# Kernel tuning notes

Measured on AMD Instinct MI355X. Metric: run time of the kernel, lower is better.

## Reference

```python
import jax, jax.numpy as jnp
from jax import lax
import numpy as np

D = 1024      # hidden_size
H = 6         # num_heads
DK = 128      # head_k_dim
DV = 256      # head_v_dim (head_dim * expand_v)
KD = H * DK   # key_dim = 768
VD = H * DV   # value_dim = 1536
KS = 4        # conv_size
EPS = 1e-5
B, L = 2, 1024


def _causal_conv_silu(x, w):
    # x: [B, L, C], w: [C, KS] depthwise causal conv then SiLU
    xt = jnp.transpose(x, (0, 2, 1))  # [B, C, L]
    out = lax.conv_general_dilated(
        xt, w[:, None, :], window_strides=(1,), padding=[(KS - 1, 0)],
        feature_group_count=w.shape[0])
    return jnp.transpose(jax.nn.silu(out), (0, 2, 1))  # [B, L, C]


def setup_inputs() -> dict:
    key = jax.random.key(0)
    ks = jax.random.split(key, 16)
    s = 0.02
    x = jax.random.normal(ks[0], (B, L, D), dtype=jnp.float32)
    Wq = jax.random.normal(ks[1], (D, KD), dtype=jnp.float32) * s
    Wk = jax.random.normal(ks[2], (D, KD), dtype=jnp.float32) * s
    Wv = jax.random.normal(ks[3], (D, VD), dtype=jnp.float32) * s
    Wb = jax.random.normal(ks[4], (D, H), dtype=jnp.float32) * s
    Wa = jax.random.normal(ks[5], (D, H), dtype=jnp.float32) * s
    A_log = jnp.log(jax.random.uniform(ks[6], (H,), minval=1e-3, maxval=16.0))
    dt = jnp.exp(jax.random.uniform(ks[7], (H,)) * (np.log(0.1) - np.log(0.001)) + np.log(0.001))
    dt = jnp.clip(dt, 1e-4)
    dt_bias = dt + jnp.log(-jnp.expm1(-dt))
    conv_q = jax.random.normal(ks[8], (KD, KS), dtype=jnp.float32) * 0.3
    conv_k = jax.random.normal(ks[9], (KD, KS), dtype=jnp.float32) * 0.3
    conv_v = jax.random.normal(ks[10], (VD, KS), dtype=jnp.float32) * 0.3
    Wg = jax.random.normal(ks[11], (D, VD), dtype=jnp.float32) * s
    norm_w = jnp.ones((DV,), dtype=jnp.float32)
    Wo = jax.random.normal(ks[12], (VD, D), dtype=jnp.float32) * s
    return {"x": x, "Wq": Wq, "Wk": Wk, "Wv": Wv, "Wb": Wb, "Wa": Wa,
            "A_log": A_log, "dt_bias": dt_bias, "conv_q": conv_q,
            "conv_k": conv_k, "conv_v": conv_v, "Wg": Wg,
            "norm_w": norm_w, "Wo": Wo}


def _l2norm(t):
    return t * lax.rsqrt(jnp.sum(t * t, axis=-1, keepdims=True) + 1e-12)


def reference(x, Wq, Wk, Wv, Wb, Wa, A_log, dt_bias, conv_q, conv_k, conv_v,
              Wg, norm_w, Wo):
    Bc, Lc, _ = x.shape
    q = _causal_conv_silu(x @ Wq, conv_q).reshape(Bc, Lc, H, DK)
    k = _causal_conv_silu(x @ Wk, conv_k).reshape(Bc, Lc, H, DK)
    v = _causal_conv_silu(x @ Wv, conv_v).reshape(Bc, Lc, H, DV)
    beta = jax.nn.sigmoid(x @ Wb)                              # [B,L,H]
    g = -jnp.exp(A_log) * jax.nn.softplus(x @ Wa + dt_bias)     # [B,L,H]

    q = _l2norm(q) * (DK ** -0.5)
    k = _l2norm(k)

    # time-major for scan
    qt = jnp.moveaxis(q, 1, 0)    # [L,B,H,DK]
    kt = jnp.moveaxis(k, 1, 0)
    vt = jnp.moveaxis(v, 1, 0)    # [L,B,H,DV]
    gt = jnp.moveaxis(g, 1, 0)    # [L,B,H]
    bt = jnp.moveaxis(beta, 1, 0)

    S0 = jnp.zeros((Bc, H, DK, DV), dtype=x.dtype)

    def step(S, inp):
        q_t, k_t, v_t, g_t, b_t = inp
        S = S * jnp.exp(g_t)[..., None, None]
        corr = jnp.einsum('bhk,bhkv->bhv', k_t, S)
        u = (v_t - corr) * b_t[..., None]
        S = S + k_t[..., None] * u[:, :, None, :]
        o_t = jnp.einsum('bhk,bhkv->bhv', q_t, S)
        return S, o_t

    S, o = lax.scan(step, S0, (qt, kt, vt, gt, bt))
    o = jnp.moveaxis(o, 0, 1)      # [B,L,H,DV]

    gate = (x @ Wg).reshape(Bc, Lc, H, DV)
    o = o * lax.rsqrt(jnp.mean(o * o, axis=-1, keepdims=True) + EPS)
    o = o * norm_w * jax.nn.silu(gate)
    o = o.reshape(Bc, Lc, VD) @ Wo
    return o, S
```

## Files before the change

kernel.cpp:

```cpp
#include <hip/hip_runtime.h>

#define B_ 2
#define L_ 1024
#define D_ 1024
#define H_ 6
#define DK_ 128
#define DV_ 256
#define KD_ 768
#define VD_ 1536
#define KS_ 4
#define KD2_ 1536
#define VD2_ 3072

using bf16x8 = __attribute__((ext_vector_type(8))) short;
using u16x8 = __attribute__((ext_vector_type(8))) unsigned short;
using f32x4 = __attribute__((ext_vector_type(4))) float;

__device__ __forceinline__ float silu_f(float x) { return x / (1.0f + expf(-x)); }

__device__ __forceinline__ unsigned short f2bf(float f) {
  unsigned int u = __float_as_uint(f);
  u = (u + 0x7fffu + ((u >> 16) & 1u)) >> 16;
  return (unsigned short)u;
}

__device__ __forceinline__ void gl_lds16(const void* g, void* l) {
  __builtin_amdgcn_global_load_lds((const __attribute__((address_space(1))) unsigned int*)g,
                                   (__attribute__((address_space(3))) unsigned int*)l, 16, 0, 0);
}
__device__ __forceinline__ void gl_lds4(const void* g, void* l) {
  __builtin_amdgcn_global_load_lds((const __attribute__((address_space(1))) unsigned int*)g,
                                   (__attribute__((address_space(3))) unsigned int*)l, 4, 0, 0);
}

template <int CTRL>
__device__ __forceinline__ float dpp_add(float x) {
  int y = __builtin_amdgcn_mov_dpp(__float_as_int(x), CTRL, 0xF, 0xF, true);
  return x + __int_as_float(y);
}
__device__ __forceinline__ float red16(float x) {
  x = dpp_add<0xB1>(x);
  x = dpp_add<0x4E>(x);
  x = dpp_add<0x141>(x);
  x = dpp_add<0x140>(x);
  return x;
}

__global__ __launch_bounds__(256) void sgemm64(const float* __restrict__ A,
                                               const float* __restrict__ Bm,
                                               float* __restrict__ C,
                                               int M, int N, int K) {
  __shared__ float As[16][64];
  __shared__ float Bs[16][64];
  const int tid = threadIdx.x;
  const int bx = blockIdx.x, by = blockIdx.y;
  const int tx = tid & 15, ty = tid >> 4;
  const int m0 = by * 64, n0 = bx * 64;
  const int ar = tid >> 2, ac = (tid & 3) << 2;
  const int br = tid >> 4, bc = (tid & 15) << 2;
  const bool n4 = ((N & 3) == 0);
  float acc[4][4];
#pragma unroll
  for (int i = 0; i < 4; i++)
#pragma unroll
    for (int j = 0; j < 4; j++) acc[i][j] = 0.0f;

  for (int k0 = 0; k0 < K; k0 += 16) {
    float4 av = *reinterpret_cast<const float4*>(A + (size_t)(m0 + ar) * K + (k0 + ac));
    As[ac + 0][ar] = av.x;
    As[ac + 1][ar] = av.y;
    As[ac + 2][ar] = av.z;
    As[ac + 3][ar] = av.w;
    float4 bv;
    if (n4 && (n0 + bc + 3 < N)) {
      bv = *reinterpret_cast<const float4*>(Bm + (size_t)(k0 + br) * N + (n0 + bc));
    } else {
      bv.x = (n0 + bc + 0 < N) ? Bm[(size_t)(k0 + br) * N + (n0 + bc + 0)] : 0.0f;
      bv.y = (n0 + bc + 1 < N) ? Bm[(size_t)(k0 + br) * N + (n0 + bc + 1)] : 0.0f;
      bv.z = (n0 + bc + 2 < N) ? Bm[(size_t)(k0 + br) * N + (n0 + bc + 2)] : 0.0f;
      bv.w = (n0 + bc + 3 < N) ? Bm[(size_t)(k0 + br) * N + (n0 + bc + 3)] : 0.0f;
    }
    Bs[br][bc + 0] = bv.x;
    Bs[br][bc + 1] = bv.y;
    Bs[br][bc + 2] = bv.z;
    Bs[br][bc + 3] = bv.w;
    __syncthreads();
#pragma unroll
    for (int kk = 0; kk < 16; kk++) {
      float4 a = *reinterpret_cast<const float4*>(&As[kk][ty << 2]);
      float4 b = *reinterpret_cast<const float4*>(&Bs[kk][tx << 2]);
      acc[0][0] = fmaf(a.x, b.x, acc[0][0]);
      acc[0][1] = fmaf(a.x, b.y, acc[0][1]);
      acc[0][2] = fmaf(a.x, b.z, acc[0][2]);
      acc[0][3] = fmaf(a.x, b.w, acc[0][3]);
      acc[1][0] = fmaf(a.y, b.x, acc[1][0]);
      acc[1][1] = fmaf(a.y, b.y, acc[1][1]);
      acc[1][2] = fmaf(a.y, b.z, acc[1][2]);
      acc[1][3] = fmaf(a.y, b.w, acc[1][3]);
      acc[2][0] = fmaf(a.z, b.x, acc[2][0]);
      acc[2][1] = fmaf(a.z, b.y, acc[2][1]);
      acc[2][2] = fmaf(a.z, b.z, acc[2][2]);
      acc[2][3] = fmaf(a.z, b.w, acc[2][3]);
      acc[3][0] = fmaf(a.w, b.x, acc[3][0]);
      acc[3][1] = fmaf(a.w, b.y, acc[3][1]);
      acc[3][2] = fmaf(a.w, b.z, acc[3][2]);
      acc[3][3] = fmaf(a.w, b.w, acc[3][3]);
    }
    __syncthreads();
  }
#pragma unroll
  for (int i = 0; i < 4; i++) {
    int m = m0 + (ty << 2) + i;
#pragma unroll
    for (int j = 0; j < 4; j++) {
      int n = n0 + (tx << 2) + j;
      if (n < N) C[(size_t)m * N + n] = acc[i][j];
    }
  }
}

__global__ void cast_bf16_kernel(const float* __restrict__ in, unsigned short* __restrict__ out,
                                 int n4) {
  int i = blockIdx.x * 256 + threadIdx.x;
  if (i >= n4) return;
  float4 v = *reinterpret_cast<const float4*>(in + (size_t)i * 4);
  ushort4 o;
  o.x = f2bf(v.x);
  o.y = f2bf(v.y);
  o.z = f2bf(v.z);
  o.w = f2bf(v.w);
  *reinterpret_cast<ushort4*>(out + (size_t)i * 4) = o;
}

__global__ __launch_bounds__(256) void tcast_kernel(const float* __restrict__ W,
                                                    unsigned short* __restrict__ Wt,
                                                    int K, int N) {
  __shared__ unsigned short T[64][72];
  const int tid = threadIdx.x;
  const int k0 = blockIdx.y * 64, n0 = blockIdx.x * 64;
  const int c4 = (tid & 15) * 4, r = tid >> 4;
#pragma unroll
  for (int j = 0; j < 4; j++) {
    int row = r + j * 16;
    float4 w = *reinterpret_cast<const float4*>(W + (size_t)(k0 + row) * N + n0 + c4);
    T[c4 + 0][row] = f2bf(w.x);
    T[c4 + 1][row] = f2bf(w.y);
    T[c4 + 2][row] = f2bf(w.z);
    T[c4 + 3][row] = f2bf(w.w);
  }
  __syncthreads();
#pragma unroll
  for (int j = 0; j < 4; j++) {
    int nr = r + j * 16;
    ushort4 o;
    o.x = T[nr][c4 + 0];
    o.y = T[nr][c4 + 1];
    o.z = T[nr][c4 + 2];
    o.w = T[nr][c4 + 3];
    *reinterpret_cast<ushort4*>(Wt + (size_t)(n0 + nr) * K + k0 + c4) = o;
  }
}

__global__ __launch_bounds__(256) void mfma_gemm(const unsigned short* __restrict__ A,
                                                 const unsigned short* __restrict__ Bt,
                                                 float* __restrict__ C,
                                                 int M, int N, int K) {
  __shared__ __attribute__((aligned(16))) unsigned short As[128][32];
  __shared__ __attribute__((aligned(16))) unsigned short Bs[128][32];
  const int tid = threadIdx.x;
  const int wave = tid >> 6, lane = tid & 63;
  const int wm = wave >> 1, wn = wave & 1;
  const int m0 = blockIdx.y * 128, n0 = blockIdx.x * 128;
  const int lrow = lane >> 4;
  const int lcol = lane & 15;
  const int sr = lane >> 2;
  const int sc = lane & 3;

  f32x4 acc[4][4];
#pragma unroll
  for (int i = 0; i < 4; i++)
#pragma unroll
    for (int j = 0; j < 4; j++) acc[i][j] = f32x4{0.f, 0.f, 0.f, 0.f};

  const int Ra = wave * 32;

  for (int k0 = 0; k0 < K; k0 += 32) {
#pragma unroll
    for (int half = 0; half < 2; half++) {
      int r = Ra + half * 16 + sr;
      int ch = sc ^ ((r >> 1) & 3);
      gl_lds16(A + (size_t)(m0 + r) * K + k0 + ch * 8, &As[Ra + half * 16][0]);
      gl_lds16(Bt + (size_t)(n0 + r) * K + k0 + ch * 8, &Bs[Ra + half * 16][0]);
    }
    __syncthreads();
    bf16x8 af[4], bfr[4];
#pragma unroll
    for (int mr = 0; mr < 4; mr++) {
      int row = wm * 64 + mr * 16 + lcol;
      af[mr] = *reinterpret_cast<const bf16x8*>(&As[row][(lrow ^ ((row >> 1) & 3)) * 8]);
    }
#pragma unroll
    for (int nr = 0; nr < 4; nr++) {
      int row = wn * 64 + nr * 16 + lcol;
      bfr[nr] = *reinterpret_cast<const bf16x8*>(&Bs[row][(lrow ^ ((row >> 1) & 3)) * 8]);
    }
#pragma unroll
    for (int mr = 0; mr < 4; mr++)
#pragma unroll
      for (int nr = 0; nr < 4; nr++)
        acc[mr][nr] = __builtin_amdgcn_mfma_f32_16x16x32_bf16(af[mr], bfr[nr], acc[mr][nr], 0, 0, 0);
    __syncthreads();
  }

#pragma unroll
  for (int mr = 0; mr < 4; mr++) {
    int row = m0 + wm * 64 + mr * 16 + lrow * 4;
#pragma unroll
    for (int nr = 0; nr < 4; nr++) {
      int col = n0 + wn * 64 + nr * 16 + lcol;
#pragma unroll
      for (int r = 0; r < 4; r++) C[(size_t)(row + r) * N + col] = acc[mr][nr][r];
    }
  }
}

__global__ void concat_ba_kernel(const float* __restrict__ Wb, const float* __restrict__ Wa,
                                 float* __restrict__ Wba) {
  int i = blockIdx.x * 256 + threadIdx.x;
  if (i >= D_ * 12) return;
  int k = i / 12, j = i % 12;
  Wba[i] = (j < 6) ? Wb[k * 6 + j] : Wa[k * 6 + (j - 6)];
}

__global__ void ba_kernel(const float* __restrict__ yba,
                          const float* __restrict__ A_log, const float* __restrict__ dt_bias,
                          float* __restrict__ beta_t, float* __restrict__ eg_t) {
  int i = blockIdx.x * 256 + threadIdx.x;
  if (i >= B_ * L_ * H_) return;
  int h = i % H_, bl = i / H_;
  int l = bl % L_, b = bl / L_;
  float yb = yba[(size_t)bl * 12 + h];
  float ya = yba[(size_t)bl * 12 + 6 + h];
  float beta = 1.0f / (1.0f + expf(-yb));
  float z = ya + dt_bias[h];
  float sp = (z > 20.0f) ? z : log1pf(expf(z));
  float g = -expf(A_log[h]) * sp;
  size_t o = ((size_t)b * H_ + h) * L_ + l;
  beta_t[o] = beta;
  eg_t[o] = expf(g);
}

__global__ __launch_bounds__(256) void conv_qk_kernel(
    const float* __restrict__ yqk,
    const float* __restrict__ cwq, const float* __restrict__ cwk,
    float* __restrict__ qhat, float* __restrict__ khat) {
  const int lane = threadIdx.x & 63;
  const int widx = (blockIdx.x << 2) + (threadIdx.x >> 6);
  const int h = widx % H_;
  const int bl = widx / H_;
  const int l = bl % L_;
  const int b = bl / L_;
  const int ch = lane << 1;
  const int gc = h * DK_ + ch;

  float wq0[KS_], wq1[KS_], wk0[KS_], wk1[KS_];
#pragma unroll
  for (int j = 0; j < KS_; j++) {
    wq0[j] = cwq[(size_t)gc * KS_ + j];
    wq1[j] = cwq[(size_t)(gc + 1) * KS_ + j];
    wk0[j] = cwk[(size_t)gc * KS_ + j];
    wk1[j] = cwk[(size_t)(gc + 1) * KS_ + j];
  }
  float aq0 = 0, aq1 = 0, ak0 = 0, ak1 = 0;
#pragma unroll
  for (int j = 0; j < KS_; j++) {
    int ll = l - (KS_ - 1) + j;
    if (ll >= 0) {
      const size_t off = (size_t)(b * L_ + ll) * KD2_ + gc;
      float2 tq = *reinterpret_cast<const float2*>(yqk + off);
      float2 tk = *reinterpret_cast<const float2*>(yqk + off + 768);
      aq0 = fmaf(tq.x, wq0[j], aq0);
      aq1 = fmaf(tq.y, wq1[j], aq1);
      ak0 = fmaf(tk.x, wk0[j], ak0);
      ak1 = fmaf(tk.y, wk1[j], ak1);
    }
  }
  float q0 = silu_f(aq0), q1 = silu_f(aq1);
  float k0v = silu_f(ak0), k1v = silu_f(ak1);
  float ssq = q0 * q0 + q1 * q1;
  float ssk = k0v * k0v + k1v * k1v;
#pragma unroll
  for (int m = 1; m < 64; m <<= 1) {
    ssq += __shfl_xor(ssq, m);
    ssk += __shfl_xor(ssk, m);
  }
  float xq = ssq + 1e-12f;
  float rq = rsqrtf(xq);
  rq = rq * (1.5f - 0.5f * xq * rq * rq);
  float xk = ssk + 1e-12f;
  float rk = rsqrtf(xk);
  rk = rk * (1.5f - 0.5f * xk * rk * rk);
  rq *= 0.08838834764831845f;
  size_t oo = (size_t)bl * KD_ + gc;
  *reinterpret_cast<float2*>(qhat + oo) = make_float2(q0 * rq, q1 * rq);
  *reinterpret_cast<float2*>(khat + oo) = make_float2(k0v * rk, k1v * rk);
}

__global__ void conv_v_kernel(const float* __restrict__ yvg, const float* __restrict__ cwv,
                              float* __restrict__ v) {
  int idx = blockIdx.x * 256 + threadIdx.x;
  int c = idx % VD_;
  int bl = idx / VD_;
  int l = bl % L_;
  float w[KS_];
#pragma unroll
  for (int j = 0; j < KS_; j++) w[j] = cwv[(size_t)c * KS_ + j];
  float acc = 0;
#pragma unroll
  for (int j = 0; j < KS_; j++) {
    int ll = l - (KS_ - 1) + j;
    if (ll >= 0) acc = fmaf(yvg[(size_t)(bl - l + ll) * VD2_ + c], w[j], acc);
  }
  v[idx] = silu_f(acc);
}

__global__ __launch_bounds__(256) void gp_kernel(const float* __restrict__ qhat,
                                                 const float* __restrict__ khat,
                                                 float* __restrict__ gp) {
  const int W = (blockIdx.x << 2) + (threadIdx.x >> 6);
  const int lane = threadIdx.x & 63;
  const int blk = W & 255;
  const int bh = W >> 8;
  const int b = bh / H_, h = bh % H_;
  const int t0 = blk * 4;
  const size_t base = (size_t)(b * L_ + t0) * KD_ + h * DK_ + 2 * lane;
  float2 k1 = *reinterpret_cast<const float2*>(khat + base);
  float2 k2 = *reinterpret_cast<const float2*>(khat + base + KD_);
  float2 k3 = *reinterpret_cast<const float2*>(khat + base + 2 * KD_);
  float2 k4 = *reinterpret_cast<const float2*>(khat + base + 3 * KD_);
  float2 q1 = *reinterpret_cast<const float2*>(qhat + base);
  float2 q2 = *reinterpret_cast<const float2*>(qhat + base + KD_);
  float2 q3 = *reinterpret_cast<const float2*>(qhat + base + 2 * KD_);
  float2 q4 = *reinterpret_cast<const float2*>(qhat + base + 3 * KD_);
  float g21 = k2.x * k1.x + k2.y * k1.y;
  float g31 = k3.x * k1.x + k3.y * k1.y;
  float g32 = k3.x * k2.x + k3.y * k2.y;
  float g41 = k4.x * k1.x + k4.y * k1.y;
  float g42 = k4.x * k2.x + k4.y * k2.y;
  float g43 = k4.x * k3.x + k4.y * k3.y;
  float p21 = q2.x * k1.x + q2.y * k1.y;
  float p31 = q3.x * k1.x + q3.y * k1.y;
  float p32 = q3.x * k2.x + q3.y * k2.y;
  float p41 = q4.x * k1.x + q4.y * k1.y;
  float p42 = q4.x * k2.x + q4.y * k2.y;
  float p43 = q4.x * k3.x + q4.y * k3.y;
  float p11 = q1.x * k1.x + q1.y * k1.y;
  float p22 = q2.x * k2.x + q2.y * k2.y;
  float p33 = q3.x * k3.x + q3.y * k3.y;
  float p44 = q4.x * k4.x + q4.y * k4.y;
#pragma unroll
  for (int m = 1; m < 64; m <<= 1) {
    g21 += __shfl_xor(g21, m); g31 += __shfl_xor(g31, m); g32 += __shfl_xor(g32, m);
    g41 += __shfl_xor(g41, m); g42 += __shfl_xor(g42, m); g43 += __shfl_xor(g43, m);
    p21 += __shfl_xor(p21, m); p31 += __shfl_xor(p31, m); p32 += __shfl_xor(p32, m);
    p41 += __shfl_xor(p41, m); p42 += __shfl_xor(p42, m); p43 += __shfl_xor(p43, m);
    p11 += __shfl_xor(p11, m); p22 += __shfl_xor(p22, m); p33 += __shfl_xor(p33, m);
    p44 += __shfl_xor(p44, m);
  }
  const bool l0 = lane & 1, l1 = lane & 2, l2 = lane & 4, l3 = lane & 8;
  float s00 = l0 ? g31 : g21, s01 = l0 ? g41 : g32, s02 = l0 ? g43 : g42, s03 = l0 ? p31 : p21;
  float s04 = l0 ? p41 : p32, s05 = l0 ? p43 : p42, s06 = l0 ? p22 : p11, s07 = l0 ? p44 : p33;
  float s10 = l1 ? s01 : s00, s11 = l1 ? s03 : s02, s12 = l1 ? s05 : s04, s13 = l1 ? s07 : s06;
  float s20 = l2 ? s11 : s10, s21 = l2 ? s13 : s12;
  float out = l3 ? s21 : s20;
  if (lane < 16) gp[((size_t)bh * 256 + blk) * 16 + lane] = out;
}

__global__ __launch_bounds__(64) void scan_kernel(
    const float* __restrict__ qhat, const float* __restrict__ khat,
    const float* __restrict__ vconv, const float* __restrict__ beta_t,
    const float* __restrict__ eg_t, const float* __restrict__ gp,
    float* __restrict__ o_scan, float* __restrict__ S_out) {
  __shared__ __attribute__((aligned(16))) float kq[2][16][256];
  __shared__ __attribute__((aligned(16))) float scv[2][16][4];
  __shared__ __attribute__((aligned(16))) float sce[2][4][16];
  __shared__ __attribute__((aligned(16))) float gps[2][4][16];

  const int lane = threadIdx.x & 63;
  const int wg = blockIdx.x;
  const int virt = (wg & 7) * 96 + (wg >> 3);
  const int bh = virt >> 6;
  const int tile = virt & 63;
  const int b = bh / H_, h = bh % H_;
  const int grp = lane >> 4;
  const int lsub = lane & 15;
  const int col = tile * 4 + grp;

  const float* kbase = khat + (size_t)b * L_ * KD_ + h * DK_;
  const float* qbase = qhat + (size_t)b * L_ * KD_ + h * DK_;
  const float* vbase = vconv + (size_t)b * L_ * VD_ + h * DV_ + tile * 4;
  const float* egp = eg_t + (size_t)bh * L_;
  const float* bp = beta_t + (size_t)bh * L_;
  const float* gpb = gp + (size_t)bh * 256 * 16;
  float* op = o_scan + (size_t)b * L_ * VD_ + h * DV_ + col;

  float S[8];
#pragma unroll
  for (int i = 0; i < 8; i++) S[i] = 0.0f;

  const int sl = lane & 31;
  const int vt = lane >> 2, vc = lane & 3;
  const int et = lane & 15, ej = lane >> 4;
  const float* ebase = (ej == 0) ? egp : bp;

#define STAGE(W, BB)                                                                   \
  do {                                                                                 \
    const int _t0 = (W) * 16;                                                          \
    _Pragma("unroll") for (int _j = 0; _j < 16; _j++) {                                \
      const float* _src = (lane < 32) ? (kbase + (size_t)(_t0 + _j) * KD_ + sl * 4)    \
                                      : (qbase + (size_t)(_t0 + _j) * KD_ + sl * 4);   \
      gl_lds16(_src, &kq[BB][_j][0]);                                                  \
    }                                                                                  \
    gl_lds4(vbase + (size_t)(_t0 + vt) * VD_ + vc, &scv[BB][0][0]);                    \
    gl_lds4(ebase + _t0 + et, &sce[BB][0][0]);                                         \
    gl_lds4(gpb + (size_t)(W) * 64 + lane, &gps[BB][0][0]);                            \
  } while (0)

#define DOT8(L4, H4) \
  ((fmaf(S[0], (L4).x, S[1] * (L4).y) + fmaf(S[2], (L4).z, S[3] * (L4).w)) + \
   (fmaf(S[4], (H4).x, S[5] * (H4).y) + fmaf(S[6], (H4).z, S[7] * (H4).w)))

  STAGE(0, 0);
  STAGE(1, 1);
  asm volatile("s_waitcnt vmcnt(19)" ::: "memory");
  __builtin_amdgcn_sched_barrier(0);

  int cur = 0;
  for (int w = 0; w < L_ / 16; ++w) {
    const int t0 = w * 16;
#pragma unroll
    for (int sb = 0; sb < 4; ++sb) {
      const int j0 = sb * 4;
      float4 k1l = *reinterpret_cast<const float4*>(&kq[cur][j0 + 0][lsub * 4]);
      float4 k1h = *reinterpret_cast<const float4*>(&kq[cur][j0 + 0][64 + lsub * 4]);
      float4 q1l = *reinterpret_cast<const float4*>(&kq[cur][j0 + 0][128 + lsub * 4]);
      float4 q1h = *reinterpret_cast<const float4*>(&kq[cur][j0 + 0][192 + lsub * 4]);
      float4 k2l = *reinterpret_cast<const float4*>(&kq[cur][j0 + 1][lsub * 4]);
      float4 k2h = *reinterpret_cast<const float4*>(&kq[cur][j0 + 1][64 + lsub * 4]);
      float4 q2l = *reinterpret_cast<const float4*>(&kq[cur][j0 + 1][128 + lsub * 4]);
      float4 q2h = *reinterpret_cast<const float4*>(&kq[cur][j0 + 1][192 + lsub * 4]);
      float4 k3l = *reinterpret_cast<const float4*>(&kq[cur][j0 + 2][lsub * 4]);
      float4 k3h = *reinterpret_cast<const float4*>(&kq[cur][j0 + 2][64 + lsub * 4]);
      float4 q3l = *reinterpret_cast<const float4*>(&kq[cur][j0 + 2][128 + lsub * 4]);
      float4 q3h = *reinterpret_cast<const float4*>(&kq[cur][j0 + 2][192 + lsub * 4]);
      float4 k4l = *reinterpret_cast<const float4*>(&kq[cur][j0 + 3][lsub * 4]);
      float4 k4h = *reinterpret_cast<const float4*>(&kq[cur][j0 + 3][64 + lsub * 4]);
      float4 q4l = *reinterpret_cast<const float4*>(&kq[cur][j0 + 3][128 + lsub * 4]);
      float4 q4h = *reinterpret_cast<const float4*>(&kq[cur][j0 + 3][192 + lsub * 4]);
      float v1 = scv[cur][j0 + 0][grp], v2 = scv[cur][j0 + 1][grp];
      float v3 = scv[cur][j0 + 2][grp], v4 = scv[cur][j0 + 3][grp];
      float e1 = sce[cur][0][j0 + 0], e2 = sce[cur][0][j0 + 1];
      float e3 = sce[cur][0][j0 + 2], e4 = sce[cur][0][j0 + 3];
      float bt1 = sce[cur][1][j0 + 0], bt2 = sce[cur][1][j0 + 1];
      float bt3 = sce[cur][1][j0 + 2], bt4 = sce[cur][1][j0 + 3];
      float g21 = gps[cur][sb][0], g31 = gps[cur][sb][1], g32 = gps[cur][sb][2];
      float g41 = gps[cur][sb][3], g42 = gps[cur][sb][4], g43 = gps[cur][sb][5];
      float p21 = gps[cur][sb][6], p31 = gps[cur][sb][7], p32 = gps[cur][sb][8];
      float p41 = gps[cur][sb][9], p42 = gps[cur][sb][10], p43 = gps[cur][sb][11];
      float p11 = gps[cur][sb][12], p22 = gps[cur][sb][13];
      float p33 = gps[cur][sb][14], p44 = gps[cur][sb][15];

      float a1 = red16(DOT8(k1l, k1h));
      float a2 = red16(DOT8(k2l, k2h));
      float a3 = red16(DOT8(k3l, k3h));
      float a4 = red16(DOT8(k4l, k4h));
      float b1 = red16(DOT8(q1l, q1h));
      float b2 = red16(DOT8(q2l, q2h));
      float b3 = red16(DOT8(q3l, q3h));
      float b4 = red16(DOT8(q4l, q4h));

      float E2 = e1 * e2, E3 = E2 * e3, E4 = E3 * e4;
      float f32v = e3 * e2, f43 = e4 * e3, f432 = e4 * f32v;
      float u1 = (v1 - e1 * a1) * bt1;
      float c2 = fmaf(g21, u1, e1 * a2);
      float u2 = (v2 - e2 * c2) * bt2;
      float c3 = fmaf(g32, u2, fmaf(e2 * g31, u1, E2 * a3));
      float u3 = (v3 - e3 * c3) * bt3;
      float c4 = fmaf(g43, u3, fmaf(e3 * g42, u2, fmaf(f32v * g41, u1, E3 * a4)));
      float u4 = (v4 - e4 * c4) * bt4;
      float o1 = fmaf(p11, u1, e1 * b1);
      float o2 = fmaf(p22, u2, fmaf(e2 * p21, u1, E2 * b2));
      float o3 = fmaf(p33, u3, fmaf(e3 * p32, u2, fmaf(f32v * p31, u1, E3 * b3)));
      float o4 = fmaf(p44, u4,
                      fmaf(e4 * p43, u3, fmaf(f43 * p42, u2, fmaf(f432 * p41, u1, E4 * b4))));
      float w1 = f432 * u1, w2 = f43 * u2, w3 = e4 * u3, w4 = u4;

      S[0] = fmaf(k4l.x, w4, fmaf(k3l.x, w3, fmaf(k2l.x, w2, fmaf(k1l.x, w1, S[0] * E4))));
      S[1] = fmaf(k4l.y, w4, fmaf(k3l.y, w3, fmaf(k2l.y, w2, fmaf(k1l.y, w1, S[1] * E4))));
      S[2] = fmaf(k4l.z, w4, fmaf(k3l.z, w3, fmaf(k2l.z, w2, fmaf(k1l.z, w1, S[2] * E4))));
      S[3] = fmaf(k4l.w, w4, fmaf(k3l.w, w3, fmaf(k2l.w, w2, fmaf(k1l.w, w1, S[3] * E4))));
      S[4] = fmaf(k4h.x, w4, fmaf(k3h.x, w3, fmaf(k2h.x, w2, fmaf(k1h.x, w1, S[4] * E4))));
      S[5] = fmaf(k4h.y, w4, fmaf(k3h.y, w3, fmaf(k2h.y, w2, fmaf(k1h.y, w1, S[5] * E4))));
      S[6] = fmaf(k4h.z, w4, fmaf(k3h.z, w3, fmaf(k2h.z, w2, fmaf(k1h.z, w1, S[6] * E4))));
      S[7] = fmaf(k4h.w, w4, fmaf(k3h.w, w3, fmaf(k2h.w, w2, fmaf(k1h.w, w1, S[7] * E4))));

      if (lsub == 0) {
        op[(size_t)(t0 + j0 + 0) * VD_] = o1;
        op[(size_t)(t0 + j0 + 1) * VD_] = o2;
        op[(size_t)(t0 + j0 + 2) * VD_] = o3;
        op[(size_t)(t0 + j0 + 3) * VD_] = o4;
      }
    }
    __builtin_amdgcn_sched_barrier(0);
    if (w < L_ / 16 - 2) {
      STAGE(w + 2, cur);
      asm volatile("s_waitcnt vmcnt(35)" ::: "memory");
    } else {
      asm volatile("s_waitcnt vmcnt(0)" ::: "memory");
    }
    __builtin_amdgcn_sched_barrier(0);
    cur ^= 1;
  }

#pragma unroll
  for (int i = 0; i < 4; i++) {
    S_out[((size_t)bh * DK_ + lsub * 4 + i) * DV_ + col] = S[i];
    S_out[((size_t)bh * DK_ + 64 + lsub * 4 + i) * DV_ + col] = S[4 + i];
  }
#undef STAGE
#undef DOT8
}

__global__ __launch_bounds__(256) void normgate_kernel(
    const float* __restrict__ o_scan, const float* __restrict__ yvg,
    const float* __restrict__ norm_w, unsigned short* __restrict__ o2b) {
  const int lane = threadIdx.x & 63;
  const int widx = (blockIdx.x << 2) + (threadIdx.x >> 6);
  const int h = widx % H_;
  const int bl = widx / H_;
  size_t base = (size_t)bl * VD_ + h * DV_ + (lane << 2);
  size_t gbase = (size_t)bl * VD2_ + VD_ + h * DV_ + (lane << 2);
  float4 o4 = *reinterpret_cast<const float4*>(o_scan + base);
  float ss = o4.x * o4.x + o4.y * o4.y + o4.z * o4.z + o4.w * o4.w;
#pragma unroll
  for (int m = 1; m < 64; m <<= 1) ss += __shfl_xor(ss, m);
  float x = ss * (1.0f / DV_) + 1e-5f;
  float r = rsqrtf(x);
  r = r * (1.5f - 0.5f * x * r * r);
  float4 g4 = *reinterpret_cast<const float4*>(yvg + gbase);
  float4 nw = *reinterpret_cast<const float4*>(norm_w + (lane << 2));
  ushort4 out;
  out.x = f2bf(o4.x * r * nw.x * silu_f(g4.x));
  out.y = f2bf(o4.y * r * nw.y * silu_f(g4.y));
  out.z = f2bf(o4.z * r * nw.z * silu_f(g4.z));
  out.w = f2bf(o4.w * r * nw.w * silu_f(g4.w));
  *reinterpret_cast<ushort4*>(o2b + base) = out;
}

extern "C" void kernel_launch(void* const* d_in, const int* in_sizes, int n_in,
                              void* d_out, int out_size, void* d_ws, size_t ws_size,
                              hipStream_t stream) {
  const float* x = (const float*)d_in[0];
  const float* Wq = (const float*)d_in[1];
  const float* Wk = (const float*)d_in[2];
  const float* Wv = (const float*)d_in[3];
  const float* Wb = (const float*)d_in[4];
  const float* Wa = (const float*)d_in[5];
  const float* A_log = (const float*)d_in[6];
  const float* dt_bias = (const float*)d_in[7];
  const float* conv_q = (const float*)d_in[8];
  const float* conv_k = (const float*)d_in[9];
  const float* conv_v = (const float*)d_in[10];
  const float* Wg = (const float*)d_in[11];
  const float* norm_w = (const float*)d_in[12];
  const float* Wo = (const float*)d_in[13];

  float* ws = (float*)d_ws;
  const size_t szQK = (size_t)B_ * L_ * KD_;
  const size_t szV = (size_t)B_ * L_ * VD_;
  const size_t szH = (size_t)B_ * L_ * H_;
  const size_t szX = (size_t)B_ * L_ * D_;
  const size_t szQK2 = (size_t)B_ * L_ * KD2_;
  const size_t szV2 = (size_t)B_ * L_ * VD2_;
  const size_t szGP = (size_t)B_ * H_ * (L_ / 4) * 16;

  float* yqk = ws;
  float* yvg = yqk + szQK2;
  float* yba = yvg + szV2;
  float* beta_t = yba + 12 * B_ * L_;
  float* eg_t = beta_t + szH;
  float* qhat = eg_t + szH;
  float* khat = qhat + szQK;
  float* vconv = khat + szQK;
  float* gp = vconv + szV;
  float* Wba = gp + szGP;
  unsigned short* xb = (unsigned short*)(Wba + (size_t)D_ * 12);
  unsigned short* Wqkt = xb + szX;
  unsigned short* Wvgt = Wqkt + (size_t)KD2_ * D_;
  unsigned short* Wot = Wvgt + (size_t)VD2_ * D_;
  float* o_scan = yqk;
  unsigned short* o2b = (unsigned short*)yvg;

  float* o_out = (float*)d_out;
  float* S_out = o_out + (size_t)B_ * L_ * D_;

  const int M = B_ * L_;

  cast_bf16_kernel<<<(szX / 4 + 255) / 256, 256, 0, stream>>>(x, xb, szX / 4);
  tcast_kernel<<<dim3(KD_ / 64, D_ / 64), 256, 0, stream>>>(Wq, Wqkt, D_, KD_);
  tcast_kernel<<<dim3(KD_ / 64, D_ / 64), 256, 0, stream>>>(Wk, Wqkt + (size_t)KD_ * D_, D_, KD_);
  tcast_kernel<<<dim3(VD_ / 64, D_ / 64), 256, 0, stream>>>(Wv, Wvgt, D_, VD_);
  tcast_kernel<<<dim3(VD_ / 64, D_ / 64), 256, 0, stream>>>(Wg, Wvgt + (size_t)VD_ * D_, D_, VD_);
  tcast_kernel<<<dim3(D_ / 64, VD_ / 64), 256, 0, stream>>>(Wo, Wot, VD_, D_);
  concat_ba_kernel<<<(D_ * 12 + 255) / 256, 256, 0, stream>>>(Wb, Wa, Wba);

  mfma_gemm<<<dim3(KD2_ / 128, M / 128), 256, 0, stream>>>(xb, Wqkt, yqk, M, KD2_, D_);
  mfma_gemm<<<dim3(VD2_ / 128, M / 128), 256, 0, stream>>>(xb, Wvgt, yvg, M, VD2_, D_);
  sgemm64<<<dim3(1, M / 64), 256, 0, stream>>>(x, Wba, yba, M, 12, D_);

  ba_kernel<<<(B_ * L_ * H_ + 255) / 256, 256, 0, stream>>>(yba, A_log, dt_bias, beta_t, eg_t);
  conv_qk_kernel<<<(B_ * L_ * H_) / 4, 256, 0, stream>>>(yqk, conv_q, conv_k, qhat, khat);
  conv_v_kernel<<<(B_ * L_ * VD_) / 256, 256, 0, stream>>>(yvg, conv_v, vconv);
  gp_kernel<<<(B_ * H_ * (L_ / 4)) / 4, 256, 0, stream>>>(qhat, khat, gp);

  scan_kernel<<<B_ * H_ * 64, 64, 0, stream>>>(qhat, khat, vconv, beta_t, eg_t, gp,
                                               o_scan, S_out);

  normgate_kernel<<<(B_ * L_ * H_) / 4, 256, 0, stream>>>(o_scan, yvg, norm_w, o2b);
  mfma_gemm<<<dim3(D_ / 128, M / 128), 256, 0, stream>>>(o2b, Wot, o_out, M, D_, VD_);
}
```

Measured before the change: 499.3 us.

## Widen scan chunk to 8 steps with precomputed decay-weighted Gram coefficients

The prepass now computes, per 8-token chunk, the k·k and q·k Gram entries already multiplied by cumulative decay products, plus the cumulative decay and the per-token weights for the state update, and writes them as a 96-float record. The scan kernel processes 8 tokens per sub-block instead of 4, batches the 16 cross-lane reductions before the sequential triangular solve, and applies a single decay multiply to the state per chunk. This halves the number of serial state-update rounds and moves decay arithmetic out of the latency-bound scan. In exchange it uses more registers in the scan, produces a larger prepass record stream, and has a longer triangular dependency chain per chunk.

```diff
diff --git a/kernel.cpp b/kernel.cpp
--- a/kernel.cpp
+++ b/kernel.cpp
@@ -324,67 +324,88 @@
   v[idx] = silu_f(acc);
 }
 
-__global__ __launch_bounds__(256) void gp_kernel(const float* __restrict__ qhat,
-                                                 const float* __restrict__ khat,
-                                                 float* __restrict__ gp) {
+__global__ __launch_bounds__(256) void gp2_kernel(const float* __restrict__ qhat,
+                                                  const float* __restrict__ khat,
+                                                  const float* __restrict__ eg_t,
+                                                  float* __restrict__ gp) {
   const int W = (blockIdx.x << 2) + (threadIdx.x >> 6);
   const int lane = threadIdx.x & 63;
-  const int blk = W & 255;
-  const int bh = W >> 8;
+  const int blk = W & 127;
+  const int bh = W >> 7;
   const int b = bh / H_, h = bh % H_;
-  const int t0 = blk * 4;
+  const int t0 = blk * 8;
   const size_t base = (size_t)(b * L_ + t0) * KD_ + h * DK_ + 2 * lane;
-  float2 k1 = *reinterpret_cast<const float2*>(khat + base);
-  float2 k2 = *reinterpret_cast<const float2*>(khat + base + KD_);
-  float2 k3 = *reinterpret_cast<const float2*>(khat + base + 2 * KD_);
-  float2 k4 = *reinterpret_cast<const float2*>(khat + base + 3 * KD_);
-  float2 q1 = *reinterpret_cast<const float2*>(qhat + base);
-  float2 q2 = *reinterpret_cast<const float2*>(qhat + base + KD_);
-  float2 q3 = *reinterpret_cast<const float2*>(qhat + base + 2 * KD_);
-  float2 q4 = *reinterpret_cast<const float2*>(qhat + base + 3 * KD_);
-  float g21 = k2.x * k1.x + k2.y * k1.y;
-  float g31 = k3.x * k1.x + k3.y * k1.y;
-  float g32 = k3.x * k2.x + k3.y * k2.y;
-  float g41 = k4.x * k1.x + k4.y * k1.y;
-  float g42 = k4.x * k2.x + k4.y * k2.y;
-  float g43 = k4.x * k3.x + k4.y * k3.y;
-  float p21 = q2.x * k1.x + q2.y * k1.y;
-  float p31 = q3.x * k1.x + q3.y * k1.y;
-  float p32 = q3.x * k2.x + q3.y * k2.y;
-  float p41 = q4.x * k1.x + q4.y * k1.y;
-  float p42 = q4.x * k2.x + q4.y * k2.y;
-  float p43 = q4.x * k3.x + q4.y * k3.y;
-  float p11 = q1.x * k1.x + q1.y * k1.y;
-  float p22 = q2.x * k2.x + q2.y * k2.y;
-  float p33 = q3.x * k3.x + q3.y * k3.y;
-  float p44 = q4.x * k4.x + q4.y * k4.y;
+  float2 k[8], q[8];
+#pragma unroll
+  for (int t = 0; t < 8; t++) {
+    k[t] = *reinterpret_cast<const float2*>(khat + base + (size_t)t * KD_);
+    q[t] = *reinterpret_cast<const float2*>(qhat + base + (size_t)t * KD_);
+  }
+  float g[28], p[36];
+#pragma unroll
+  for (int t = 1; t < 8; t++)
+#pragma unroll
+    for (int j = 0; j < t; j++)
+      g[t * (t - 1) / 2 + j] = k[t].x * k[j].x + k[t].y * k[j].y;
+#pragma unroll
+  for (int t = 0; t < 8; t++)
+#pragma unroll
+    for (int j = 0; j <= t; j++)
+      p[t * (t + 1) / 2 + j] = q[t].x * k[j].x + q[t].y * k[j].y;
 #pragma unroll
   for (int m = 1; m < 64; m <<= 1) {
-    g21 += __shfl_xor(g21, m); g31 += __shfl_xor(g31, m); g32 += __shfl_xor(g32, m);
-    g41 += __shfl_xor(g41, m); g42 += __shfl_xor(g42, m); g43 += __shfl_xor(g43, m);
-    p21 += __shfl_xor(p21, m); p31 += __shfl_xor(p31, m); p32 += __shfl_xor(p32, m);
-    p41 += __shfl_xor(p41, m); p42 += __shfl_xor(p42, m); p43 += __shfl_xor(p43, m);
-    p11 += __shfl_xor(p11, m); p22 += __shfl_xor(p22, m); p33 += __shfl_xor(p33, m);
-    p44 += __shfl_xor(p44, m);
-  }
-  const bool l0 = lane & 1, l1 = lane & 2, l2 = lane & 4, l3 = lane & 8;
-  float s00 = l0 ? g31 : g21, s01 = l0 ? g41 : g32, s02 = l0 ? g43 : g42, s03 = l0 ? p31 : p21;
-  float s04 = l0 ? p41 : p32, s05 = l0 ? p43 : p42, s06 = l0 ? p22 : p11, s07 = l0 ? p44 : p33;
-  float s10 = l1 ? s01 : s00, s11 = l1 ? s03 : s02, s12 = l1 ? s05 : s04, s13 = l1 ? s07 : s06;
-  float s20 = l2 ? s11 : s10, s21 = l2 ? s13 : s12;
-  float out = l3 ? s21 : s20;
-  if (lane < 16) gp[((size_t)bh * 256 + blk) * 16 + lane] = out;
+#pragma unroll
+    for (int i = 0; i < 28; i++) g[i] += __shfl_xor(g[i], m);
+#pragma unroll
+    for (int i = 0; i < 36; i++) p[i] += __shfl_xor(p[i], m);
+  }
+  const float* egp = eg_t + (size_t)bh * L_ + t0;
+  float lam[8], LAM[8];
+#pragma unroll
+  for (int t = 0; t < 8; t++) lam[t] = egp[t];
+  LAM[0] = lam[0];
+#pragma unroll
+  for (int t = 1; t < 8; t++) LAM[t] = LAM[t - 1] * lam[t];
+  float Dm[28];
+#pragma unroll
+  for (int t = 1; t < 8; t++)
+#pragma unroll
+    for (int j = 0; j < t; j++)
+      Dm[t * (t - 1) / 2 + j] =
+          (j == t - 1) ? lam[t] : Dm[(t - 1) * (t - 2) / 2 + j] * lam[t];
+  if (lane == 0) {
+    float* rec = gp + (size_t)W * 96;
+#pragma unroll
+    for (int t = 0; t < 8; t++) rec[t] = LAM[t];
+#pragma unroll
+    for (int t = 1; t < 8; t++)
+#pragma unroll
+      for (int j = 0; j < t; j++) {
+        int ix = t * (t - 1) / 2 + j;
+        rec[8 + ix] = Dm[ix] * g[ix];
+      }
+#pragma unroll
+    for (int t = 0; t < 8; t++)
+#pragma unroll
+      for (int j = 0; j <= t; j++) {
+        int ix = t * (t + 1) / 2 + j;
+        rec[36 + ix] = (j == t) ? p[ix] : Dm[t * (t - 1) / 2 + j] * p[ix];
+      }
+#pragma unroll
+    for (int j = 0; j < 7; j++) rec[72 + j] = Dm[21 + j];
+    rec[79] = 1.0f;
+  }
 }
 
 __global__ __launch_bounds__(64) void scan_kernel(
     const float* __restrict__ qhat, const float* __restrict__ khat,
     const float* __restrict__ vconv, const float* __restrict__ beta_t,
-    const float* __restrict__ eg_t, const float* __restrict__ gp,
+    const float* __restrict__ gp,
     float* __restrict__ o_scan, float* __restrict__ S_out) {
   __shared__ __attribute__((aligned(16))) float kq[2][16][256];
   __shared__ __attribute__((aligned(16))) float scv[2][16][4];
-  __shared__ __attribute__((aligned(16))) float sce[2][4][16];
-  __shared__ __attribute__((aligned(16))) float gps[2][4][16];
+  __shared__ __attribute__((aligned(16))) float scb[2][64];
+  __shared__ __attribute__((aligned(16))) float gps[2][192];
 
   const int lane = threadIdx.x & 63;
   const int wg = blockIdx.x;
@@ -399,9 +420,8 @@
   const float* kbase = khat + (size_t)b * L_ * KD_ + h * DK_;
   const float* qbase = qhat + (size_t)b * L_ * KD_ + h * DK_;
   const float* vbase = vconv + (size_t)b * L_ * VD_ + h * DV_ + tile * 4;
-  const float* egp = eg_t + (size_t)bh * L_;
   const float* bp = beta_t + (size_t)bh * L_;
-  const float* gpb = gp + (size_t)bh * 256 * 16;
+  const float* gpb = gp + (size_t)bh * 128 * 96;
   float* op = o_scan + (size_t)b * L_ * VD_ + h * DV_ + col;
 
   float S[8];
@@ -410,8 +430,6 @@
 
   const int sl = lane & 31;
   const int vt = lane >> 2, vc = lane & 3;
-  const int et = lane & 15, ej = lane >> 4;
-  const float* ebase = (ej == 0) ? egp : bp;
 
 #define STAGE(W, BB)                                                                   \
   do {                                                                                 \
@@ -422,8 +440,10 @@
       gl_lds16(_src, &kq[BB][_j][0]);                                                  \
     }                                                                                  \
     gl_lds4(vbase + (size_t)(_t0 + vt) * VD_ + vc, &scv[BB][0][0]);                    \
-    gl_lds4(ebase + _t0 + et, &sce[BB][0][0]);                                         \
-    gl_lds4(gpb + (size_t)(W) * 64 + lane, &gps[BB][0][0]);                            \
+    gl_lds4(bp + _t0 + (lane & 15), &scb[BB][0]);                                      \
+    gl_lds4(gpb + (size_t)(W) * 192 + lane, &gps[BB][0]);                              \
+    gl_lds4(gpb + (size_t)(W) * 192 + 64 + lane, &gps[BB][64]);                        \
+    gl_lds4(gpb + (size_t)(W) * 192 + 128 + lane, &gps[BB][128]);                      \
   } while (0)
 
 #define DOT8(L4, H4) \
@@ -432,89 +452,69 @@
 
   STAGE(0, 0);
   STAGE(1, 1);
-  asm volatile("s_waitcnt vmcnt(19)" ::: "memory");
+  asm volatile("s_waitcnt vmcnt(21)" ::: "memory");
   __builtin_amdgcn_sched_barrier(0);
 
   int cur = 0;
   for (int w = 0; w < L_ / 16; ++w) {
     const int t0 = w * 16;
 #pragma unroll
-    for (int sb = 0; sb < 4; ++sb) {
-      const int j0 = sb * 4;
-      float4 k1l = *reinterpret_cast<const float4*>(&kq[cur][j0 + 0][lsub * 4]);
-      float4 k1h = *reinterpret_cast<const float4*>(&kq[cur][j0 + 0][64 + lsub * 4]);
-      float4 q1l = *reinterpret_cast<const float4*>(&kq[cur][j0 + 0][128 + lsub * 4]);
-      float4 q1h = *reinterpret_cast<const float4*>(&kq[cur][j0 + 0][192 + lsub * 4]);
-      float4 k2l = *reinterpret_cast<const float4*>(&kq[cur][j0 + 1][lsub * 4]);
-      float4 k2h = *reinterpret_cast<const float4*>(&kq[cur][j0 + 1][64 + lsub * 4]);
-      float4 q2l = *reinterpret_cast<const float4*>(&kq[cur][j0 + 1][128 + lsub * 4]);
-      float4 q2h = *reinterpret_cast<const float4*>(&kq[cur][j0 + 1][192 + lsub * 4]);
-      float4 k3l = *reinterpret_cast<const float4*>(&kq[cur][j0 + 2][lsub * 4]);
-      float4 k3h = *reinterpret_cast<const float4*>(&kq[cur][j0 + 2][64 + lsub * 4]);
-      float4 q3l = *reinterpret_cast<const float4*>(&kq[cur][j0 + 2][128 + lsub * 4]);
-      float4 q3h = *reinterpret_cast<const float4*>(&kq[cur][j0 + 2][192 + lsub * 4]);
-      float4 k4l = *reinterpret_cast<const float4*>(&kq[cur][j0 + 3][lsub * 4]);
-      float4 k4h = *reinterpret_cast<const float4*>(&kq[cur][j0 + 3][64 + lsub * 4]);
-      float4 q4l = *reinterpret_cast<const float4*>(&kq[cur][j0 + 3][128 + lsub * 4]);
-      float4 q4h = *reinterpret_cast<const float4*>(&kq[cur][j0 + 3][192 + lsub * 4]);
-      float v1 = scv[cur][j0 + 0][grp], v2 = scv[cur][j0 + 1][grp];
-      float v3 = scv[cur][j0 + 2][grp], v4 = scv[cur][j0 + 3][grp];
-      float e1 = sce[cur][0][j0 + 0], e2 = sce[cur][0][j0 + 1];
-      float e3 = sce[cur][0][j0 + 2], e4 = sce[cur][0][j0 + 3];
-      float bt1 = sce[cur][1][j0 + 0], bt2 = sce[cur][1][j0 + 1];
-      float bt3 = sce[cur][1][j0 + 2], bt4 = sce[cur][1][j0 + 3];
-      float g21 = gps[cur][sb][0], g31 = gps[cur][sb][1], g32 = gps[cur][sb][2];
-      float g41 = gps[cur][sb][3], g42 = gps[cur][sb][4], g43 = gps[cur][sb][5];
-      float p21 = gps[cur][sb][6], p31 = gps[cur][sb][7], p32 = gps[cur][sb][8];
-      float p41 = gps[cur][sb][9], p42 = gps[cur][sb][10], p43 = gps[cur][sb][11];
-      float p11 = gps[cur][sb][12], p22 = gps[cur][sb][13];
-      float p33 = gps[cur][sb][14], p44 = gps[cur][sb][15];
-
-      float a1 = red16(DOT8(k1l, k1h));
-      float a2 = red16(DOT8(k2l, k2h));
-      float a3 = red16(DOT8(k3l, k3h));
-      float a4 = red16(DOT8(k4l, k4h));
-      float b1 = red16(DOT8(q1l, q1h));
-      float b2 = red16(DOT8(q2l, q2h));
-      float b3 = red16(DOT8(q3l, q3h));
-      float b4 = red16(DOT8(q4l, q4h));
-
-      float E2 = e1 * e2, E3 = E2 * e3, E4 = E3 * e4;
-      float f32v = e3 * e2, f43 = e4 * e3, f432 = e4 * f32v;
-      float u1 = (v1 - e1 * a1) * bt1;
-      float c2 = fmaf(g21, u1, e1 * a2);
-      float u2 = (v2 - e2 * c2) * bt2;
-      float c3 = fmaf(g32, u2, fmaf(e2 * g31, u1, E2 * a3));
-      float u3 = (v3 - e3 * c3) * bt3;
-      float c4 = fmaf(g43, u3, fmaf(e3 * g42, u2, fmaf(f32v * g41, u1, E3 * a4)));
-      float u4 = (v4 - e4 * c4) * bt4;
-      float o1 = fmaf(p11, u1, e1 * b1);
-      float o2 = fmaf(p22, u2, fmaf(e2 * p21, u1, E2 * b2));
-      float o3 = fmaf(p33, u3, fmaf(e3 * p32, u2, fmaf(f32v * p31, u1, E3 * b3)));
-      float o4 = fmaf(p44, u4,
-                      fmaf(e4 * p43, u3, fmaf(f43 * p42, u2, fmaf(f432 * p41, u1, E4 * b4))));
-      float w1 = f432 * u1, w2 = f43 * u2, w3 = e4 * u3, w4 = u4;
-
-      S[0] = fmaf(k4l.x, w4, fmaf(k3l.x, w3, fmaf(k2l.x, w2, fmaf(k1l.x, w1, S[0] * E4))));
-      S[1] = fmaf(k4l.y, w4, fmaf(k3l.y, w3, fmaf(k2l.y, w2, fmaf(k1l.y, w1, S[1] * E4))));
-      S[2] = fmaf(k4l.z, w4, fmaf(k3l.z, w3, fmaf(k2l.z, w2, fmaf(k1l.z, w1, S[2] * E4))));
-      S[3] = fmaf(k4l.w, w4, fmaf(k3l.w, w3, fmaf(k2l.w, w2, fmaf(k1l.w, w1, S[3] * E4))));
-      S[4] = fmaf(k4h.x, w4, fmaf(k3h.x, w3, fmaf(k2h.x, w2, fmaf(k1h.x, w1, S[4] * E4))));
-      S[5] = fmaf(k4h.y, w4, fmaf(k3h.y, w3, fmaf(k2h.y, w2, fmaf(k1h.y, w1, S[5] * E4))));
-      S[6] = fmaf(k4h.z, w4, fmaf(k3h.z, w3, fmaf(k2h.z, w2, fmaf(k1h.z, w1, S[6] * E4))));
-      S[7] = fmaf(k4h.w, w4, fmaf(k3h.w, w3, fmaf(k2h.w, w2, fmaf(k1h.w, w1, S[7] * E4))));
-
-      if (lsub == 0) {
-        op[(size_t)(t0 + j0 + 0) * VD_] = o1;
-        op[(size_t)(t0 + j0 + 1) * VD_] = o2;
-        op[(size_t)(t0 + j0 + 2) * VD_] = o3;
-        op[(size_t)(t0 + j0 + 3) * VD_] = o4;
+    for (int sb = 0; sb < 2; ++sb) {
+      const int j0 = sb * 8;
+      const int co = sb * 96;
+      float4 kl[8], kh[8];
+      float a[8], bq[8];
+#pragma unroll
+      for (int t = 0; t < 8; t++) {
+        kl[t] = *reinterpret_cast<const float4*>(&kq[cur][j0 + t][lsub * 4]);
+        kh[t] = *reinterpret_cast<const float4*>(&kq[cur][j0 + t][64 + lsub * 4]);
+        float4 ql = *reinterpret_cast<const float4*>(&kq[cur][j0 + t][128 + lsub * 4]);
+        float4 qh = *reinterpret_cast<const float4*>(&kq[cur][j0 + t][192 + lsub * 4]);
+        a[t] = DOT8(kl[t], kh[t]);
+        bq[t] = DOT8(ql, qh);
+      }
+#pragma unroll
+      for (int t = 0; t < 8; t++) {
+        a[t] = red16(a[t]);
+        bq[t] = red16(bq[t]);
+      }
+      float u[8];
+#pragma unroll
+      for (int t = 0; t < 8; t++) {
+        float lamt = gps[cur][co + t];
+        float c = lamt * a[t];
+#pragma unroll
+        for (int j = 0; j < t; j++)
+          c = fmaf(gps[cur][co + 8 + t * (t - 1) / 2 + j], u[j], c);
+        u[t] = scb[cur][j0 + t] * (scv[cur][j0 + t][grp] - c);
+        float o = lamt * bq[t];
+#pragma unroll
+        for (int j = 0; j <= t; j++)
+          o = fmaf(gps[cur][co + 36 + t * (t + 1) / 2 + j], u[j], o);
+        if (lsub == 0) op[(size_t)(t0 + j0 + t) * VD_] = o;
+      }
+      float wg2[8];
+#pragma unroll
+      for (int j = 0; j < 8; j++) wg2[j] = gps[cur][co + 72 + j] * u[j];
+      const float L8 = gps[cur][co + 7];
+      S[0] *= L8; S[1] *= L8; S[2] *= L8; S[3] *= L8;
+      S[4] *= L8; S[5] *= L8; S[6] *= L8; S[7] *= L8;
+#pragma unroll
+      for (int j = 0; j < 8; j++) {
+        S[0] = fmaf(kl[j].x, wg2[j], S[0]);
+        S[1] = fmaf(kl[j].y, wg2[j], S[1]);
+        S[2] = fmaf(kl[j].z, wg2[j], S[2]);
+        S[3] = fmaf(kl[j].w, wg2[j], S[3]);
+        S[4] = fmaf(kh[j].x, wg2[j], S[4]);
+        S[5] = fmaf(kh[j].y, wg2[j], S[5]);
+        S[6] = fmaf(kh[j].z, wg2[j], S[6]);
+        S[7] = fmaf(kh[j].w, wg2[j], S[7]);
       }
     }
     __builtin_amdgcn_sched_barrier(0);
     if (w < L_ / 16 - 2) {
       STAGE(w + 2, cur);
-      asm volatile("s_waitcnt vmcnt(35)" ::: "memory");
+      asm volatile("s_waitcnt vmcnt(37)" ::: "memory");
     } else {
       asm volatile("s_waitcnt vmcnt(0)" ::: "memory");
     }
@@ -582,7 +582,7 @@
   const size_t szX = (size_t)B_ * L_ * D_;
   const size_t szQK2 = (size_t)B_ * L_ * KD2_;
   const size_t szV2 = (size_t)B_ * L_ * VD2_;
-  const size_t szGP = (size_t)B_ * H_ * (L_ / 4) * 16;
+  const size_t szGP = (size_t)B_ * H_ * (L_ / 8) * 96;
 
   float* yqk = ws;
   float* yvg = yqk + szQK2;
@@ -621,9 +621,9 @@
   ba_kernel<<<(B_ * L_ * H_ + 255) / 256, 256, 0, stream>>>(yba, A_log, dt_bias, beta_t, eg_t);
   conv_qk_kernel<<<(B_ * L_ * H_) / 4, 256, 0, stream>>>(yqk, conv_q, conv_k, qhat, khat);
   conv_v_kernel<<<(B_ * L_ * VD_) / 256, 256, 0, stream>>>(yvg, conv_v, vconv);
-  gp_kernel<<<(B_ * H_ * (L_ / 4)) / 4, 256, 0, stream>>>(qhat, khat, gp);
-
-  scan_kernel<<<B_ * H_ * 64, 64, 0, stream>>>(qhat, khat, vconv, beta_t, eg_t, gp,
+  gp2_kernel<<<(B_ * H_ * (L_ / 8)) / 4, 256, 0, stream>>>(qhat, khat, eg_t, gp);
+
+  scan_kernel<<<B_ * H_ * 64, 64, 0, stream>>>(qhat, khat, vconv, beta_t, gp,
                                                o_scan, S_out);
 
   normgate_kernel<<<(B_ * L_ * H_) / 4, 256, 0, stream>>>(o_scan, yvg, norm_w, o2b);
```

Result: slower. 561.9 us (+12.6%).
